# Kernel tuning notes

Measured on AMD Instinct MI355X. Metric: run time of the kernel, lower is better.

## Reference

```python
import jax, jax.numpy as jnp
from jax import lax
import numpy as np

B, T, F, H, L = 256, 512, 64, 128, 2


def lstm_layer(x, W_ih, W_hh, b_ih, b_hh):
    """PyTorch-style LSTM layer. x:[B,T,I]; W_ih:[4H,I]; W_hh:[4H,H]. Gate order i,f,g,o."""
    b = x.shape[0]
    h_dim = W_hh.shape[1]
    # Precompute input contribution for all timesteps: [B,T,4H]
    xg = jnp.einsum('bti,gi->btg', x, W_ih) + b_ih + b_hh

    def step(carry, xg_t):
        h, c = carry
        g = xg_t + h @ W_hh.T  # [B,4H]
        i, f, gg, o = jnp.split(g, 4, axis=-1)
        c = jax.nn.sigmoid(f) * c + jax.nn.sigmoid(i) * jnp.tanh(gg)
        h = jax.nn.sigmoid(o) * jnp.tanh(c)
        return (h, c), h

    h0 = jnp.zeros((b, h_dim), x.dtype)
    c0 = jnp.zeros((b, h_dim), x.dtype)
    (hT, _), hs = lax.scan(step, (h0, c0), jnp.swapaxes(xg, 0, 1))  # hs:[T,B,H]
    return jnp.swapaxes(hs, 0, 1), hT


def setup_inputs() -> dict:
    key = jax.random.key(0)
    ks = iter(jax.random.split(key, 32))
    s = 0.05
    d = {"x": jax.random.normal(next(ks), (B, T, F), jnp.float32)}
    # encoder: layer0 input F, layer1 input H; decoder: both layers input H
    for name, in0 in (("enc", F), ("dec", H)):
        for l in range(L):
            I = in0 if l == 0 else H
            d[f"{name}{l}_Wih"] = jax.random.normal(next(ks), (4 * H, I), jnp.float32) * s
            d[f"{name}{l}_Whh"] = jax.random.normal(next(ks), (4 * H, H), jnp.float32) * s
            d[f"{name}{l}_bih"] = jax.random.normal(next(ks), (4 * H,), jnp.float32) * s
            d[f"{name}{l}_bhh"] = jax.random.normal(next(ks), (4 * H,), jnp.float32) * s
    d["W_out"] = jax.random.normal(next(ks), (F, H), jnp.float32) * s
    d["b_out"] = jnp.zeros((F,), jnp.float32)
    return d


def reference(x,
              enc0_Wih, enc0_Whh, enc0_bih, enc0_bhh,
              enc1_Wih, enc1_Whh, enc1_bih, enc1_bhh,
              dec0_Wih, dec0_Whh, dec0_bih, dec0_bhh,
              dec1_Wih, dec1_Whh, dec1_bih, dec1_bhh,
              W_out, b_out):
    enc = [(enc0_Wih, enc0_Whh, enc0_bih, enc0_bhh),
           (enc1_Wih, enc1_Whh, enc1_bih, enc1_bhh)]
    dec = [(dec0_Wih, dec0_Whh, dec0_bih, dec0_bhh),
           (dec1_Wih, dec1_Whh, dec1_bih, dec1_bhh)]
    # Encoder: stacked LSTM, keep last layer's final hidden state
    h = x
    hT = None
    for p in enc:
        h, hT = lstm_layer(h, *p)
    # Repeat final hidden over sequence
    dec_in = jnp.broadcast_to(hT[:, None, :], (x.shape[0], x.shape[1], hT.shape[-1]))
    # Decoder: stacked LSTM over full output sequence
    d = dec_in
    for p in dec:
        d, _ = lstm_layer(d, *p)
    # Linear projection back to feature space
    return jnp.einsum('bth,fh->btf', d, W_out) + b_out
```

## Files before the change

kernel.cpp:

```cpp
#include <hip/hip_runtime.h>
#include <cstddef>

namespace {

typedef _Float16 half_t;
typedef _Float16 half2_t __attribute__((ext_vector_type(2)));
typedef _Float16 f16x4 __attribute__((ext_vector_type(4)));
typedef _Float16 f16x8 __attribute__((ext_vector_type(8)));
typedef float f32x4 __attribute__((ext_vector_type(4)));

constexpr int NB = 256;
constexpr int NT = 512;
constexpr int NH = 128;
constexpr int NG = 512;

__device__ __forceinline__ float sigm(float x) { return 1.0f / (1.0f + __expf(-x)); }
__device__ __forceinline__ float tanh_(float x) { return 2.0f / (1.0f + __expf(-2.0f * x)) - 1.0f; }
__device__ __forceinline__ float dot4(float4 w, float4 v, float acc) {
  return fmaf(w.x, v.x, fmaf(w.y, v.y, fmaf(w.z, v.z, fmaf(w.w, v.w, acc))));
}
__device__ __forceinline__ float fdot2(half2_t a, half2_t b, float c) {
  return __builtin_amdgcn_fdot2(a, b, c, false);
}
__device__ __forceinline__ void pinv8(f16x8& x) { asm volatile("" : "+v"(x)); }

__device__ __forceinline__ float qreduce(float v) {
  int t = __builtin_amdgcn_update_dpp(0, __float_as_int(v), 0xB1, 0xF, 0xF, true);
  v += __int_as_float(t);
  t = __builtin_amdgcn_update_dpp(0, __float_as_int(v), 0x4E, 0xF, 0xF, true);
  return v + __int_as_float(t);
}

__global__ void cvt_kernel(const float* __restrict__ s, half_t* __restrict__ d, int n4) {
  int i = blockIdx.x * blockDim.x + threadIdx.x;
  if (i < n4) {
    float4 v = reinterpret_cast<const float4*>(s)[i];
    f16x4 hv = {(half_t)v.x, (half_t)v.y, (half_t)v.z, (half_t)v.w};
    reinterpret_cast<f16x4*>(d)[i] = hv;
  }
}

template <int K, bool AF32, bool F32OUT>
__global__ __launch_bounds__(256) void xg_gemm(
    const void* __restrict__ Ap, const float* __restrict__ Bw,
    const float* __restrict__ b0, const float* __restrict__ b1,
    half_t* __restrict__ Ch, float* __restrict__ Cf, int Nstr)
{
  __shared__ __align__(16) half_t Atile[128 * K];
  __shared__ __align__(16) half_t Btile[64 * K];
  const int tid = threadIdx.x;
  const int m0 = blockIdx.x * 128;
  const int n0 = blockIdx.y * 64;
  char* Ab = (char*)Atile;
  char* Bb = (char*)Btile;

  if (AF32) {
    const float* Af = (const float*)Ap;
    for (int idx = tid; idx < 128 * K / 4; idx += 256) {
      int row = idx / (K / 4), o = idx % (K / 4);
      float4 v = *(const float4*)(Af + (size_t)(m0 + row) * K + 4 * o);
      f16x4 hv = {(half_t)v.x, (half_t)v.y, (half_t)v.z, (half_t)v.w};
      int byte = ((row * K + 4 * o) * 2) ^ ((row & 7) << 4);
      *(f16x4*)(Ab + byte) = hv;
    }
  } else {
    const half_t* Ah = (const half_t*)Ap;
    for (int idx = tid; idx < 128 * K / 8; idx += 256) {
      int row = idx / (K / 8), o = idx % (K / 8);
      uint4 v = *(const uint4*)(Ah + (size_t)(m0 + row) * K + 8 * o);
      int byte = ((row * K + 8 * o) * 2) ^ ((row & 7) << 4);
      *(uint4*)(Ab + byte) = v;
    }
  }
  for (int idx = tid; idx < 64 * K / 4; idx += 256) {
    int row = idx / (K / 4), o = idx % (K / 4);
    int n = n0 + row;
    int src_row = F32OUT ? n : ((n & 3) * 128 + (n >> 2));
    float4 v = *(const float4*)(Bw + (size_t)src_row * K + 4 * o);
    f16x4 hv = {(half_t)v.x, (half_t)v.y, (half_t)v.z, (half_t)v.w};
    int byte = ((row * K + 4 * o) * 2) ^ ((row & 7) << 4);
    *(f16x4*)(Bb + byte) = hv;
  }
  __syncthreads();

  const int lane = tid & 63, w = tid >> 6;
  const int r16 = lane & 15, koff = (lane >> 4) * 8;
  f32x4 acc[2][4];
#pragma unroll
  for (int fm = 0; fm < 2; ++fm)
#pragma unroll
    for (int fn = 0; fn < 4; ++fn) acc[fm][fn] = (f32x4){0.f, 0.f, 0.f, 0.f};

#pragma unroll
  for (int ks = 0; ks < K / 32; ++ks) {
    f16x8 a[2], bf[4];
#pragma unroll
    for (int fm = 0; fm < 2; ++fm) {
      int row = w * 32 + fm * 16 + r16;
      int byte = ((row * K + ks * 32 + koff) * 2) ^ ((row & 7) << 4);
      a[fm] = *(const f16x8*)(Ab + byte);
    }
#pragma unroll
    for (int fn = 0; fn < 4; ++fn) {
      int row = fn * 16 + r16;
      int byte = ((row * K + ks * 32 + koff) * 2) ^ ((row & 7) << 4);
      bf[fn] = *(const f16x8*)(Bb + byte);
    }
#pragma unroll
    for (int fm = 0; fm < 2; ++fm)
#pragma unroll
      for (int fn = 0; fn < 4; ++fn)
        acc[fm][fn] = __builtin_amdgcn_mfma_f32_16x16x32_f16(a[fm], bf[fn], acc[fm][fn], 0, 0, 0);
  }

#pragma unroll
  for (int fm = 0; fm < 2; ++fm)
#pragma unroll
    for (int fn = 0; fn < 4; ++fn) {
      int n = n0 + fn * 16 + r16;
      int bidx = F32OUT ? n : ((n & 3) * 128 + (n >> 2));
      float bb = (b0 ? b0[bidx] : 0.f) + (b1 ? b1[bidx] : 0.f);
#pragma unroll
      for (int q = 0; q < 4; ++q) {
        int m = m0 + w * 32 + fm * 16 + (lane >> 4) * 4 + q;
        float val = acc[fm][fn][q] + bb;
        if (F32OUT) Cf[(size_t)m * Nstr + n] = val;
        else        Ch[(size_t)m * NG + n] = (half_t)val;
      }
    }
}

template <int MODE>
__global__ __attribute__((amdgpu_flat_work_group_size(512, 512)))
__attribute__((amdgpu_waves_per_eu(2, 2))) void rec_kernel(
    const half_t* __restrict__ xg,
    const float* __restrict__ hT_in,
    const float* __restrict__ WihD,
    const float* __restrict__ bih, const float* __restrict__ bhh,
    const half_t* __restrict__ Whh,
    half_t* __restrict__ seq_out,
    float* __restrict__ hT_out)
{
  const int b = blockIdx.x;
  const int tid = threadIdx.x;
  const int j = tid >> 2;
  const int kq = tid & 3;

  __shared__ __align__(16) half_t hbuf[2][4][48];
  __shared__ float xgc[NG];
  __shared__ float hinf[NH];

  f16x8 wh8[4][4];
#pragma unroll
  for (int gi = 0; gi < 4; ++gi) {
    const f16x8* p = reinterpret_cast<const f16x8*>(Whh + (size_t)(gi * NH + j) * NH + kq * 32);
#pragma unroll
    for (int r = 0; r < 4; ++r) wh8[gi][r] = p[r];
  }
#pragma unroll
  for (int gi = 0; gi < 4; ++gi)
#pragma unroll
    for (int r = 0; r < 4; ++r) pinv8(wh8[gi][r]);

  if (tid < NH) hbuf[0][tid >> 5][tid & 31] = (half_t)0.0f;
  float c = 0.0f;

  float cxi = 0.f, cxf = 0.f, cxg = 0.f, cxo = 0.f;
  if (MODE == 2) {
    if (tid < NH) hinf[tid] = hT_in[(size_t)b * NH + tid];
    __syncthreads();
    float a0 = bih[tid] + bhh[tid], a1 = 0.f, a2 = 0.f, a3 = 0.f;
    const float4* wr = (const float4*)(WihD + (size_t)tid * NH);
    const float4* hv = (const float4*)hinf;
#pragma unroll
    for (int k = 0; k < 8; ++k) {
      a0 = dot4(wr[4 * k + 0], hv[4 * k + 0], a0);
      a1 = dot4(wr[4 * k + 1], hv[4 * k + 1], a1);
      a2 = dot4(wr[4 * k + 2], hv[4 * k + 2], a2);
      a3 = dot4(wr[4 * k + 3], hv[4 * k + 3], a3);
    }
    xgc[tid] = (a0 + a1) + (a2 + a3);
    __syncthreads();
    cxi = xgc[j]; cxf = xgc[j + 128]; cxg = xgc[j + 256]; cxo = xgc[j + 384];
  }

  const half_t* xbase = nullptr;
  f16x4 xqA = {}, xqB = {};
  if (MODE != 2) {
    xbase = xg + ((size_t)b * NT) * NG + (j << 2);
    xqA = *(const f16x4*)(xbase);
    xqB = *(const f16x4*)(xbase + NG);
  }

  __syncthreads();

  auto stepf = [&](int t, int p, f16x4& xq) {
    f16x4 cur = xq;
    if (MODE != 2 && t + 2 < NT)
      xq = *(const f16x4*)(xbase + (size_t)(t + 2) * NG);

    const f16x8* hv8 = reinterpret_cast<const f16x8*>(&hbuf[p][kq][0]);

    float pa[4], pb[4];
    if (MODE == 2) {
      pa[0] = cxi * 0.25f; pa[1] = cxf * 0.25f; pa[2] = cxg * 0.25f; pa[3] = cxo * 0.25f;
    } else {
#pragma unroll
      for (int gi = 0; gi < 4; ++gi) pa[gi] = (float)cur[gi] * 0.25f;
    }
#pragma unroll
    for (int gi = 0; gi < 4; ++gi) pb[gi] = 0.f;

#pragma unroll
    for (int r8 = 0; r8 < 4; ++r8) {
      const f16x8 H = hv8[r8];
      const half2_t h0 = __builtin_shufflevector(H, H, 0, 1);
      const half2_t h1 = __builtin_shufflevector(H, H, 2, 3);
      const half2_t h2 = __builtin_shufflevector(H, H, 4, 5);
      const half2_t h3 = __builtin_shufflevector(H, H, 6, 7);
#pragma unroll
      for (int gi = 0; gi < 4; ++gi) {
        const f16x8 W = wh8[gi][r8];
        float sa = pa[gi], sb = pb[gi];
        sa = fdot2(__builtin_shufflevector(W, W, 0, 1), h0, sa);
        sb = fdot2(__builtin_shufflevector(W, W, 2, 3), h1, sb);
        sa = fdot2(__builtin_shufflevector(W, W, 4, 5), h2, sa);
        sb = fdot2(__builtin_shufflevector(W, W, 6, 7), h3, sb);
        pa[gi] = sa; pb[gi] = sb;
      }
    }
    const float a0 = qreduce(pa[0] + pb[0]);
    const float a1 = qreduce(pa[1] + pb[1]);
    const float a2 = qreduce(pa[2] + pb[2]);
    const float a3 = qreduce(pa[3] + pb[3]);

    const float ig = sigm(a0);
    const float fg = sigm(a1);
    const float gg = tanh_(a2);
    const float og = sigm(a3);
    c = fmaf(fg, c, ig * gg);
    const float h = og * tanh_(c);

    if (kq == 0) {
      hbuf[p ^ 1][j >> 5][j & 31] = (half_t)h;
      if (MODE != 1) seq_out[((size_t)b * NT + t) * NH + j] = (half_t)h;
      else if (t == NT - 1) hT_out[(size_t)b * NH + j] = h;
    }
    __syncthreads();
  };

#pragma unroll 1
  for (int t = 0; t < NT; t += 2) {
    stepf(t, 0, xqA);
    stepf(t + 1, 1, xqB);
  }
}

}

extern "C" void kernel_launch(void* const* d_in, const int* in_sizes, int n_in,
                              void* d_out, int out_size, void* d_ws, size_t ws_size,
                              hipStream_t stream) {
  (void)in_sizes; (void)n_in; (void)out_size; (void)ws_size;

  const float* x     = (const float*)d_in[0];
  const float* e0Wih = (const float*)d_in[1];
  const float* e0Whh = (const float*)d_in[2];
  const float* e0bih = (const float*)d_in[3];
  const float* e0bhh = (const float*)d_in[4];
  const float* e1Wih = (const float*)d_in[5];
  const float* e1Whh = (const float*)d_in[6];
  const float* e1bih = (const float*)d_in[7];
  const float* e1bhh = (const float*)d_in[8];
  const float* d0Wih = (const float*)d_in[9];
  const float* d0Whh = (const float*)d_in[10];
  const float* d0bih = (const float*)d_in[11];
  const float* d0bhh = (const float*)d_in[12];
  const float* d1Wih = (const float*)d_in[13];
  const float* d1Whh = (const float*)d_in[14];
  const float* d1bih = (const float*)d_in[15];
  const float* d1bhh = (const float*)d_in[16];
  const float* Wout  = (const float*)d_in[17];
  const float* bout  = (const float*)d_in[18];
  float* out = (float*)d_out;

  half_t* whh0 = (half_t*)d_ws;
  half_t* whh1 = whh0 + 512 * 128;
  half_t* whh2 = whh1 + 512 * 128;
  half_t* whh3 = whh2 + 512 * 128;
  half_t* seqA = whh3 + 512 * 128;
  half_t* xgb  = seqA + (size_t)NB * NT * NH;
  float*  hT   = (float*)(xgb + (size_t)NB * NT * NG);

  cvt_kernel<<<64, 256, 0, stream>>>(e0Whh, whh0, 512 * 128 / 4);
  cvt_kernel<<<64, 256, 0, stream>>>(e1Whh, whh1, 512 * 128 / 4);
  cvt_kernel<<<64, 256, 0, stream>>>(d0Whh, whh2, 512 * 128 / 4);
  cvt_kernel<<<64, 256, 0, stream>>>(d1Whh, whh3, 512 * 128 / 4);

  const int M = NB * NT;
  dim3 gX(M / 128, NG / 64), gP(M / 128, 1), blkG(256);
  dim3 gR(NB), blkR(512);

  xg_gemm<64, true, false><<<gX, blkG, 0, stream>>>(x, e0Wih, e0bih, e0bhh, xgb, nullptr, NG);
  rec_kernel<0><<<gR, blkR, 0, stream>>>(xgb, nullptr, nullptr, nullptr, nullptr, whh0, seqA, nullptr);

  xg_gemm<128, false, false><<<gX, blkG, 0, stream>>>(seqA, e1Wih, e1bih, e1bhh, xgb, nullptr, NG);
  rec_kernel<1><<<gR, blkR, 0, stream>>>(xgb, nullptr, nullptr, nullptr, nullptr, whh1, nullptr, hT);

  rec_kernel<2><<<gR, blkR, 0, stream>>>(nullptr, hT, d0Wih, d0bih, d0bhh, whh2, seqA, nullptr);

  xg_gemm<128, false, false><<<gX, blkG, 0, stream>>>(seqA, d1Wih, d1bih, d1bhh, xgb, nullptr, NG);
  rec_kernel<0><<<gR, blkR, 0, stream>>>(xgb, nullptr, nullptr, nullptr, nullptr, whh3, seqA, nullptr);

  xg_gemm<128, false, true><<<gP, blkG, 0, stream>>>(seqA, Wout, bout, nullptr, nullptr, out, 64);
}
```

Before: 1.861 ms.

## Fuse stacked LSTM layers into one wavefront-pipelined recurrent kernel

Merges layer 0 and layer 1 of each stack into a single recurrent kernel that runs layer 1 one timestep behind layer 0. Each step computes layer 1's input projection in-kernel from layer 0's hidden state in shared memory, so the intermediate sequence write, the xg GEMM and two launches per stack go away. Each thread now holds 32 more f16x8 weight registers and does more dot-product work per step. This raises register pressure and lengthens the serial critical path of each step, with one extra step for the drain.

```diff
diff --git a/kernel.cpp b/kernel.cpp
--- a/kernel.cpp
+++ b/kernel.cpp
@@ -130,14 +130,17 @@
     }
 }
 
-template <int MODE>
+template <bool DEC>
 __global__ __attribute__((amdgpu_flat_work_group_size(512, 512)))
-__attribute__((amdgpu_waves_per_eu(2, 2))) void rec_kernel(
-    const half_t* __restrict__ xg,
+__attribute__((amdgpu_waves_per_eu(2, 2))) void rec_fused(
+    const half_t* __restrict__ xg0,
     const float* __restrict__ hT_in,
-    const float* __restrict__ WihD,
-    const float* __restrict__ bih, const float* __restrict__ bhh,
-    const half_t* __restrict__ Whh,
+    const float* __restrict__ Wih0_32,
+    const float* __restrict__ b0a, const float* __restrict__ b0b,
+    const half_t* __restrict__ Whh0,
+    const half_t* __restrict__ WhhC,
+    const half_t* __restrict__ WihC,
+    const float* __restrict__ b1a, const float* __restrict__ b1b,
     half_t* __restrict__ seq_out,
     float* __restrict__ hT_out)
 {
@@ -146,31 +149,55 @@
   const int j = tid >> 2;
   const int kq = tid & 3;
 
-  __shared__ __align__(16) half_t hbuf[2][4][48];
+  __shared__ __align__(16) half_t h0buf[2][4][48];
+  __shared__ __align__(16) half_t h1buf[2][4][48];
   __shared__ float xgc[NG];
   __shared__ float hinf[NH];
 
-  f16x8 wh8[4][4];
+  f16x8 wh0[4][4];
 #pragma unroll
   for (int gi = 0; gi < 4; ++gi) {
-    const f16x8* p = reinterpret_cast<const f16x8*>(Whh + (size_t)(gi * NH + j) * NH + kq * 32);
-#pragma unroll
-    for (int r = 0; r < 4; ++r) wh8[gi][r] = p[r];
+    const f16x8* p = reinterpret_cast<const f16x8*>(Whh0 + (size_t)(gi * NH + j) * NH + kq * 32);
+#pragma unroll
+    for (int r = 0; r < 4; ++r) wh0[gi][r] = p[r];
   }
 #pragma unroll
   for (int gi = 0; gi < 4; ++gi)
 #pragma unroll
-    for (int r = 0; r < 4; ++r) pinv8(wh8[gi][r]);
-
-  if (tid < NH) hbuf[0][tid >> 5][tid & 31] = (half_t)0.0f;
-  float c = 0.0f;
-
-  float cxi = 0.f, cxf = 0.f, cxg = 0.f, cxo = 0.f;
-  if (MODE == 2) {
+    for (int r = 0; r < 4; ++r) pinv8(wh0[gi][r]);
+
+  f16x8 wc[4][8];
+  const half_t* cbase = (kq < 2) ? WhhC : WihC;
+#pragma unroll
+  for (int gi = 0; gi < 4; ++gi) {
+    const f16x8* p =
+        reinterpret_cast<const f16x8*>(cbase + (size_t)(gi * NH + j) * NH + (kq & 1) * 64);
+#pragma unroll
+    for (int r = 0; r < 8; ++r) wc[gi][r] = p[r];
+  }
+#pragma unroll
+  for (int gi = 0; gi < 4; ++gi)
+#pragma unroll
+    for (int r = 0; r < 8; ++r) pinv8(wc[gi][r]);
+
+  float b1g[4];
+#pragma unroll
+  for (int gi = 0; gi < 4; ++gi)
+    b1g[gi] = (b1a[gi * NH + j] + b1b[gi * NH + j]) * 0.25f;
+
+  if (tid < NH) {
+    h0buf[1][tid >> 5][tid & 31] = (half_t)0.f;
+    h1buf[1][tid >> 5][tid & 31] = (half_t)0.f;
+  }
+
+  float c0 = 0.f, c1 = 0.f;
+  float cx[4] = {0.f, 0.f, 0.f, 0.f};
+
+  if (DEC) {
     if (tid < NH) hinf[tid] = hT_in[(size_t)b * NH + tid];
     __syncthreads();
-    float a0 = bih[tid] + bhh[tid], a1 = 0.f, a2 = 0.f, a3 = 0.f;
-    const float4* wr = (const float4*)(WihD + (size_t)tid * NH);
+    float a0 = b0a[tid] + b0b[tid], a1 = 0.f, a2 = 0.f, a3 = 0.f;
+    const float4* wr = (const float4*)(Wih0_32 + (size_t)tid * NH);
     const float4* hv = (const float4*)hinf;
 #pragma unroll
     for (int k = 0; k < 8; ++k) {
@@ -181,79 +208,129 @@
     }
     xgc[tid] = (a0 + a1) + (a2 + a3);
     __syncthreads();
-    cxi = xgc[j]; cxf = xgc[j + 128]; cxg = xgc[j + 256]; cxo = xgc[j + 384];
+    cx[0] = xgc[j] * 0.25f;       cx[1] = xgc[j + 128] * 0.25f;
+    cx[2] = xgc[j + 256] * 0.25f; cx[3] = xgc[j + 384] * 0.25f;
   }
 
   const half_t* xbase = nullptr;
   f16x4 xqA = {}, xqB = {};
-  if (MODE != 2) {
-    xbase = xg + ((size_t)b * NT) * NG + (j << 2);
+  if (!DEC) {
+    xbase = xg0 + (size_t)b * NT * NG + (j << 2);
     xqA = *(const f16x4*)(xbase);
     xqB = *(const f16x4*)(xbase + NG);
   }
 
   __syncthreads();
 
-  auto stepf = [&](int t, int p, f16x4& xq) {
-    f16x4 cur = xq;
-    if (MODE != 2 && t + 2 < NT)
-      xq = *(const f16x4*)(xbase + (size_t)(t + 2) * NG);
-
-    const f16x8* hv8 = reinterpret_cast<const f16x8*>(&hbuf[p][kq][0]);
-
-    float pa[4], pb[4];
-    if (MODE == 2) {
-      pa[0] = cxi * 0.25f; pa[1] = cxf * 0.25f; pa[2] = cxg * 0.25f; pa[3] = cxo * 0.25f;
-    } else {
-#pragma unroll
-      for (int gi = 0; gi < 4; ++gi) pa[gi] = (float)cur[gi] * 0.25f;
-    }
-#pragma unroll
-    for (int gi = 0; gi < 4; ++gi) pb[gi] = 0.f;
-
-#pragma unroll
-    for (int r8 = 0; r8 < 4; ++r8) {
-      const f16x8 H = hv8[r8];
-      const half2_t h0 = __builtin_shufflevector(H, H, 0, 1);
-      const half2_t h1 = __builtin_shufflevector(H, H, 2, 3);
-      const half2_t h2 = __builtin_shufflevector(H, H, 4, 5);
-      const half2_t h3 = __builtin_shufflevector(H, H, 6, 7);
-#pragma unroll
-      for (int gi = 0; gi < 4; ++gi) {
-        const f16x8 W = wh8[gi][r8];
-        float sa = pa[gi], sb = pb[gi];
-        sa = fdot2(__builtin_shufflevector(W, W, 0, 1), h0, sa);
-        sb = fdot2(__builtin_shufflevector(W, W, 2, 3), h1, sb);
-        sa = fdot2(__builtin_shufflevector(W, W, 4, 5), h2, sa);
-        sb = fdot2(__builtin_shufflevector(W, W, 6, 7), h3, sb);
-        pa[gi] = sa; pb[gi] = sb;
-      }
-    }
-    const float a0 = qreduce(pa[0] + pb[0]);
-    const float a1 = qreduce(pa[1] + pb[1]);
-    const float a2 = qreduce(pa[2] + pb[2]);
-    const float a3 = qreduce(pa[3] + pb[3]);
-
-    const float ig = sigm(a0);
-    const float fg = sigm(a1);
-    const float gg = tanh_(a2);
-    const float og = sigm(a3);
-    c = fmaf(fg, c, ig * gg);
-    const float h = og * tanh_(c);
-
-    if (kq == 0) {
-      hbuf[p ^ 1][j >> 5][j & 31] = (half_t)h;
-      if (MODE != 1) seq_out[((size_t)b * NT + t) * NH + j] = (half_t)h;
-      else if (t == NT - 1) hT_out[(size_t)b * NH + j] = h;
+  auto stepf = [&](int s, f16x4& xq) {
+    if (s < NT) {
+      f16x4 cur = xq;
+      if (!DEC && s + 2 < NT)
+        xq = *(const f16x4*)(xbase + (size_t)(s + 2) * NG);
+
+      float pa[4], pb[4];
+      if (DEC) {
+#pragma unroll
+        for (int gi = 0; gi < 4; ++gi) pa[gi] = cx[gi];
+      } else {
+#pragma unroll
+        for (int gi = 0; gi < 4; ++gi) pa[gi] = (float)cur[gi] * 0.25f;
+      }
+#pragma unroll
+      for (int gi = 0; gi < 4; ++gi) pb[gi] = 0.f;
+
+      const f16x8* hv8 = reinterpret_cast<const f16x8*>(&h0buf[(s + 1) & 1][kq][0]);
+#pragma unroll
+      for (int r8 = 0; r8 < 4; ++r8) {
+        const f16x8 H = hv8[r8];
+        const half2_t h0 = __builtin_shufflevector(H, H, 0, 1);
+        const half2_t h1 = __builtin_shufflevector(H, H, 2, 3);
+        const half2_t h2 = __builtin_shufflevector(H, H, 4, 5);
+        const half2_t h3 = __builtin_shufflevector(H, H, 6, 7);
+#pragma unroll
+        for (int gi = 0; gi < 4; ++gi) {
+          const f16x8 W = wh0[gi][r8];
+          float sa = pa[gi], sb = pb[gi];
+          sa = fdot2(__builtin_shufflevector(W, W, 0, 1), h0, sa);
+          sb = fdot2(__builtin_shufflevector(W, W, 2, 3), h1, sb);
+          sa = fdot2(__builtin_shufflevector(W, W, 4, 5), h2, sa);
+          sb = fdot2(__builtin_shufflevector(W, W, 6, 7), h3, sb);
+          pa[gi] = sa; pb[gi] = sb;
+        }
+      }
+      const float a0 = qreduce(pa[0] + pb[0]);
+      const float a1 = qreduce(pa[1] + pb[1]);
+      const float a2 = qreduce(pa[2] + pb[2]);
+      const float a3 = qreduce(pa[3] + pb[3]);
+
+      const float ig = sigm(a0), fg = sigm(a1), gg = tanh_(a2), og = sigm(a3);
+      c0 = fmaf(fg, c0, ig * gg);
+      const float hh0 = og * tanh_(c0);
+      if (kq == 0) h0buf[s & 1][j >> 5][j & 31] = (half_t)hh0;
+    }
+
+    if (s >= 1) {
+      const half_t* cA = (kq < 2) ? &h1buf[s & 1][2 * (kq & 1)][0]
+                                  : &h0buf[(s + 1) & 1][2 * (kq & 1)][0];
+      const f16x8* A8 = reinterpret_cast<const f16x8*>(cA);
+      const f16x8* B8 = reinterpret_cast<const f16x8*>(cA + 48);
+
+      float pc[4], pd[4];
+#pragma unroll
+      for (int gi = 0; gi < 4; ++gi) { pc[gi] = b1g[gi]; pd[gi] = 0.f; }
+
+#pragma unroll
+      for (int r8 = 0; r8 < 4; ++r8) {
+        const f16x8 HA = A8[r8];
+        const f16x8 HB = B8[r8];
+        const half2_t a0p = __builtin_shufflevector(HA, HA, 0, 1);
+        const half2_t a1p = __builtin_shufflevector(HA, HA, 2, 3);
+        const half2_t a2p = __builtin_shufflevector(HA, HA, 4, 5);
+        const half2_t a3p = __builtin_shufflevector(HA, HA, 6, 7);
+        const half2_t b0p = __builtin_shufflevector(HB, HB, 0, 1);
+        const half2_t b1p = __builtin_shufflevector(HB, HB, 2, 3);
+        const half2_t b2p = __builtin_shufflevector(HB, HB, 4, 5);
+        const half2_t b3p = __builtin_shufflevector(HB, HB, 6, 7);
+#pragma unroll
+        for (int gi = 0; gi < 4; ++gi) {
+          const f16x8 WA = wc[gi][r8];
+          const f16x8 WB = wc[gi][r8 + 4];
+          float sc = pc[gi], sd = pd[gi];
+          sc = fdot2(__builtin_shufflevector(WA, WA, 0, 1), a0p, sc);
+          sd = fdot2(__builtin_shufflevector(WB, WB, 0, 1), b0p, sd);
+          sc = fdot2(__builtin_shufflevector(WA, WA, 2, 3), a1p, sc);
+          sd = fdot2(__builtin_shufflevector(WB, WB, 2, 3), b1p, sd);
+          sc = fdot2(__builtin_shufflevector(WA, WA, 4, 5), a2p, sc);
+          sd = fdot2(__builtin_shufflevector(WB, WB, 4, 5), b2p, sd);
+          sc = fdot2(__builtin_shufflevector(WA, WA, 6, 7), a3p, sc);
+          sd = fdot2(__builtin_shufflevector(WB, WB, 6, 7), b3p, sd);
+          pc[gi] = sc; pd[gi] = sd;
+        }
+      }
+      const float a0 = qreduce(pc[0] + pd[0]);
+      const float a1 = qreduce(pc[1] + pd[1]);
+      const float a2 = qreduce(pc[2] + pd[2]);
+      const float a3 = qreduce(pc[3] + pd[3]);
+
+      const float ig = sigm(a0), fg = sigm(a1), gg = tanh_(a2), og = sigm(a3);
+      c1 = fmaf(fg, c1, ig * gg);
+      const float hh1 = og * tanh_(c1);
+
+      if (kq == 0) {
+        h1buf[(s + 1) & 1][j >> 5][j & 31] = (half_t)hh1;
+        if (DEC) seq_out[((size_t)b * NT + (s - 1)) * NH + j] = (half_t)hh1;
+        else if (s == NT) hT_out[(size_t)b * NH + j] = hh1;
+      }
     }
     __syncthreads();
   };
 
 #pragma unroll 1
-  for (int t = 0; t < NT; t += 2) {
-    stepf(t, 0, xqA);
-    stepf(t + 1, 1, xqB);
-  }
+  for (int s = 0; s < NT; s += 2) {
+    stepf(s, xqA);
+    stepf(s + 1, xqB);
+  }
+  stepf(NT, xqA);
 }
 
 }
@@ -284,33 +361,36 @@
   const float* bout  = (const float*)d_in[18];
   float* out = (float*)d_out;
 
-  half_t* whh0 = (half_t*)d_ws;
-  half_t* whh1 = whh0 + 512 * 128;
-  half_t* whh2 = whh1 + 512 * 128;
-  half_t* whh3 = whh2 + 512 * 128;
-  half_t* seqA = whh3 + 512 * 128;
-  half_t* xgb  = seqA + (size_t)NB * NT * NH;
-  float*  hT   = (float*)(xgb + (size_t)NB * NT * NG);
-
-  cvt_kernel<<<64, 256, 0, stream>>>(e0Whh, whh0, 512 * 128 / 4);
-  cvt_kernel<<<64, 256, 0, stream>>>(e1Whh, whh1, 512 * 128 / 4);
-  cvt_kernel<<<64, 256, 0, stream>>>(d0Whh, whh2, 512 * 128 / 4);
-  cvt_kernel<<<64, 256, 0, stream>>>(d1Whh, whh3, 512 * 128 / 4);
+  half_t* whh0h = (half_t*)d_ws;
+  half_t* whh1h = whh0h + 512 * 128;
+  half_t* wih1h = whh1h + 512 * 128;
+  half_t* whh2h = wih1h + 512 * 128;
+  half_t* whh3h = whh2h + 512 * 128;
+  half_t* wih3h = whh3h + 512 * 128;
+  half_t* seqA  = wih3h + 512 * 128;
+  half_t* xg0   = seqA + (size_t)NB * NT * NH;
+  float*  hT    = (float*)(xg0 + (size_t)NB * NT * NG);
+
+  cvt_kernel<<<64, 256, 0, stream>>>(e0Whh, whh0h, 512 * 128 / 4);
+  cvt_kernel<<<64, 256, 0, stream>>>(e1Whh, whh1h, 512 * 128 / 4);
+  cvt_kernel<<<64, 256, 0, stream>>>(e1Wih, wih1h, 512 * 128 / 4);
+  cvt_kernel<<<64, 256, 0, stream>>>(d0Whh, whh2h, 512 * 128 / 4);
+  cvt_kernel<<<64, 256, 0, stream>>>(d1Whh, whh3h, 512 * 128 / 4);
+  cvt_kernel<<<64, 256, 0, stream>>>(d1Wih, wih3h, 512 * 128 / 4);
 
   const int M = NB * NT;
   dim3 gX(M / 128, NG / 64), gP(M / 128, 1), blkG(256);
   dim3 gR(NB), blkR(512);
 
-  xg_gemm<64, true, false><<<gX, blkG, 0, stream>>>(x, e0Wih, e0bih, e0bhh, xgb, nullptr, NG);
-  rec_kernel<0><<<gR, blkR, 0, stream>>>(xgb, nullptr, nullptr, nullptr, nullptr, whh0, seqA, nullptr);
-
-  xg_gemm<128, false, false><<<gX, blkG, 0, stream>>>(seqA, e1Wih, e1bih, e1bhh, xgb, nullptr, NG);
-  rec_kernel<1><<<gR, blkR, 0, stream>>>(xgb, nullptr, nullptr, nullptr, nullptr, whh1, nullptr, hT);
-
-  rec_kernel<2><<<gR, blkR, 0, stream>>>(nullptr, hT, d0Wih, d0bih, d0bhh, whh2, seqA, nullptr);
-
-  xg_gemm<128, false, false><<<gX, blkG, 0, stream>>>(seqA, d1Wih, d1bih, d1bhh, xgb, nullptr, NG);
-  rec_kernel<0><<<gR, blkR, 0, stream>>>(xgb, nullptr, nullptr, nullptr, nullptr, whh3, seqA, nullptr);
+  xg_gemm<64, true, false><<<gX, blkG, 0, stream>>>(x, e0Wih, e0bih, e0bhh, xg0, nullptr, NG);
+
+  rec_fused<false><<<gR, blkR, 0, stream>>>(xg0, nullptr, nullptr, nullptr, nullptr,
+                                            whh0h, whh1h, wih1h, e1bih, e1bhh,
+                                            nullptr, hT);
+
+  rec_fused<true><<<gR, blkR, 0, stream>>>(nullptr, hT, d0Wih, d0bih, d0bhh,
+                                           whh2h, whh3h, wih3h, d1bih, d1bhh,
+                                           seqA, nullptr);
 
   xg_gemm<128, false, true><<<gP, blkG, 0, stream>>>(seqA, Wout, bout, nullptr, nullptr, out, 64);
 }
```

Result: faster. 1.790 ms (-3.8%).

## Split LSTM recurrent dot products across 8 lanes with 1024-thread blocks

Applied to the files above, without the earlier changes.

The recurrent kernel now uses 1024 threads per batch row, so each hidden unit's four gate dot products are split across 8 lanes of 16 elements instead of 4 lanes of 32. A third DPP step is added to the reduction, and the bias pre-scaling changes to 1/8 so it still sums correctly. This halves the per-thread FMA chain and register weight footprint on the serial critical path, at the cost of an extra cross-lane reduction step and more wave synchronisation per timestep. A large dummy LDS pad forces one block per CU.

```diff
diff --git a/kernel.cpp b/kernel.cpp
--- a/kernel.cpp
+++ b/kernel.cpp
@@ -24,10 +24,12 @@
 }
 __device__ __forceinline__ void pinv8(f16x8& x) { asm volatile("" : "+v"(x)); }
 
-__device__ __forceinline__ float qreduce(float v) {
+__device__ __forceinline__ float r8sum(float v) {
   int t = __builtin_amdgcn_update_dpp(0, __float_as_int(v), 0xB1, 0xF, 0xF, true);
   v += __int_as_float(t);
   t = __builtin_amdgcn_update_dpp(0, __float_as_int(v), 0x4E, 0xF, 0xF, true);
+  v += __int_as_float(t);
+  t = __builtin_amdgcn_update_dpp(0, __float_as_int(v), 0x141, 0xF, 0xF, true);
   return v + __int_as_float(t);
 }
 
@@ -131,8 +133,8 @@
 }
 
 template <int MODE>
-__global__ __attribute__((amdgpu_flat_work_group_size(512, 512)))
-__attribute__((amdgpu_waves_per_eu(2, 2))) void rec_kernel(
+__global__ __attribute__((amdgpu_flat_work_group_size(1024, 1024)))
+__attribute__((amdgpu_waves_per_eu(4, 4))) void rec_kernel(
     const half_t* __restrict__ xg,
     const float* __restrict__ hT_in,
     const float* __restrict__ WihD,
@@ -143,45 +145,52 @@
 {
   const int b = blockIdx.x;
   const int tid = threadIdx.x;
-  const int j = tid >> 2;
-  const int kq = tid & 3;
-
-  __shared__ __align__(16) half_t hbuf[2][4][48];
+  const int j = tid >> 3;
+  const int ko = tid & 7;
+
+  __shared__ __align__(16) half_t hbuf[2][NH];
   __shared__ float xgc[NG];
   __shared__ float hinf[NH];
-
-  f16x8 wh8[4][4];
+  __shared__ char fpad[85 * 1024];
+
+  { volatile char* vp = fpad; vp[tid] = 0; }
+
+  f16x8 wh8[4][2];
 #pragma unroll
   for (int gi = 0; gi < 4; ++gi) {
-    const f16x8* p = reinterpret_cast<const f16x8*>(Whh + (size_t)(gi * NH + j) * NH + kq * 32);
-#pragma unroll
-    for (int r = 0; r < 4; ++r) wh8[gi][r] = p[r];
-  }
-#pragma unroll
-  for (int gi = 0; gi < 4; ++gi)
-#pragma unroll
-    for (int r = 0; r < 4; ++r) pinv8(wh8[gi][r]);
-
-  if (tid < NH) hbuf[0][tid >> 5][tid & 31] = (half_t)0.0f;
+    const f16x8* p = reinterpret_cast<const f16x8*>(Whh + (size_t)(gi * NH + j) * NH + ko * 16);
+    wh8[gi][0] = p[0];
+    wh8[gi][1] = p[1];
+  }
+#pragma unroll
+  for (int gi = 0; gi < 4; ++gi) {
+    pinv8(wh8[gi][0]);
+    pinv8(wh8[gi][1]);
+  }
+
+  if (tid < NH) hbuf[0][tid] = (half_t)0.0f;
   float c = 0.0f;
 
-  float cxi = 0.f, cxf = 0.f, cxg = 0.f, cxo = 0.f;
+  float cx[4] = {0.f, 0.f, 0.f, 0.f};
   if (MODE == 2) {
     if (tid < NH) hinf[tid] = hT_in[(size_t)b * NH + tid];
     __syncthreads();
-    float a0 = bih[tid] + bhh[tid], a1 = 0.f, a2 = 0.f, a3 = 0.f;
-    const float4* wr = (const float4*)(WihD + (size_t)tid * NH);
-    const float4* hv = (const float4*)hinf;
-#pragma unroll
-    for (int k = 0; k < 8; ++k) {
-      a0 = dot4(wr[4 * k + 0], hv[4 * k + 0], a0);
-      a1 = dot4(wr[4 * k + 1], hv[4 * k + 1], a1);
-      a2 = dot4(wr[4 * k + 2], hv[4 * k + 2], a2);
-      a3 = dot4(wr[4 * k + 3], hv[4 * k + 3], a3);
-    }
-    xgc[tid] = (a0 + a1) + (a2 + a3);
+    if (tid < NG) {
+      float a0 = bih[tid] + bhh[tid], a1 = 0.f, a2 = 0.f, a3 = 0.f;
+      const float4* wr = (const float4*)(WihD + (size_t)tid * NH);
+      const float4* hv = (const float4*)hinf;
+#pragma unroll
+      for (int k = 0; k < 8; ++k) {
+        a0 = dot4(wr[4 * k + 0], hv[4 * k + 0], a0);
+        a1 = dot4(wr[4 * k + 1], hv[4 * k + 1], a1);
+        a2 = dot4(wr[4 * k + 2], hv[4 * k + 2], a2);
+        a3 = dot4(wr[4 * k + 3], hv[4 * k + 3], a3);
+      }
+      xgc[tid] = (a0 + a1) + (a2 + a3);
+    }
     __syncthreads();
-    cxi = xgc[j]; cxf = xgc[j + 128]; cxg = xgc[j + 256]; cxo = xgc[j + 384];
+    cx[0] = xgc[j] * 0.125f;       cx[1] = xgc[j + 128] * 0.125f;
+    cx[2] = xgc[j + 256] * 0.125f; cx[3] = xgc[j + 384] * 0.125f;
   }
 
   const half_t* xbase = nullptr;
@@ -199,20 +208,21 @@
     if (MODE != 2 && t + 2 < NT)
       xq = *(const f16x4*)(xbase + (size_t)(t + 2) * NG);
 
-    const f16x8* hv8 = reinterpret_cast<const f16x8*>(&hbuf[p][kq][0]);
+    const f16x8* hv8 = reinterpret_cast<const f16x8*>(&hbuf[p][ko * 16]);
 
     float pa[4], pb[4];
     if (MODE == 2) {
-      pa[0] = cxi * 0.25f; pa[1] = cxf * 0.25f; pa[2] = cxg * 0.25f; pa[3] = cxo * 0.25f;
+#pragma unroll
+      for (int gi = 0; gi < 4; ++gi) pa[gi] = cx[gi];
     } else {
 #pragma unroll
-      for (int gi = 0; gi < 4; ++gi) pa[gi] = (float)cur[gi] * 0.25f;
+      for (int gi = 0; gi < 4; ++gi) pa[gi] = (float)cur[gi] * 0.125f;
     }
 #pragma unroll
     for (int gi = 0; gi < 4; ++gi) pb[gi] = 0.f;
 
 #pragma unroll
-    for (int r8 = 0; r8 < 4; ++r8) {
+    for (int r8 = 0; r8 < 2; ++r8) {
       const f16x8 H = hv8[r8];
       const half2_t h0 = __builtin_shufflevector(H, H, 0, 1);
       const half2_t h1 = __builtin_shufflevector(H, H, 2, 3);
@@ -229,10 +239,10 @@
         pa[gi] = sa; pb[gi] = sb;
       }
     }
-    const float a0 = qreduce(pa[0] + pb[0]);
-    const float a1 = qreduce(pa[1] + pb[1]);
-    const float a2 = qreduce(pa[2] + pb[2]);
-    const float a3 = qreduce(pa[3] + pb[3]);
+    const float a0 = r8sum(pa[0] + pb[0]);
+    const float a1 = r8sum(pa[1] + pb[1]);
+    const float a2 = r8sum(pa[2] + pb[2]);
+    const float a3 = r8sum(pa[3] + pb[3]);
 
     const float ig = sigm(a0);
     const float fg = sigm(a1);
@@ -241,8 +251,8 @@
     c = fmaf(fg, c, ig * gg);
     const float h = og * tanh_(c);
 
-    if (kq == 0) {
-      hbuf[p ^ 1][j >> 5][j & 31] = (half_t)h;
+    if (ko == 0) {
+      hbuf[p ^ 1][j] = (half_t)h;
       if (MODE != 1) seq_out[((size_t)b * NT + t) * NH + j] = (half_t)h;
       else if (t == NT - 1) hT_out[(size_t)b * NH + j] = h;
     }
@@ -299,7 +309,7 @@
 
   const int M = NB * NT;
   dim3 gX(M / 128, NG / 64), gP(M / 128, 1), blkG(256);
-  dim3 gR(NB), blkR(512);
+  dim3 gR(NB), blkR(1024);
 
   xg_gemm<64, true, false><<<gX, blkG, 0, stream>>>(x, e0Wih, e0bih, e0bhh, xgb, nullptr, NG);
   rec_kernel<0><<<gR, blkR, 0, stream>>>(xgb, nullptr, nullptr, nullptr, nullptr, whh0, seqA, nullptr);
```

After: 2.656 ms. 1.43x slower.
